# Performance work log

Hardware: AMD Instinct MI355X
Metric: run time of the kernel (lower is better)

The kernel has to match this reference:

```python
import jax, jax.numpy as jnp
import numpy as np

B, T, D, H, L = 65536, 8, 60, 128, 64


def _lstm_layer(x, Wih, Whh, bih, bhh):
    """Single LSTM layer, batch_first. x: [B,T,Din]. Returns (ys [B,T,H], h_last [B,H]).
    PyTorch gate order: i, f, g, o."""
    Bsz = x.shape[0]
    Hd = Whh.shape[1]
    # Precompute input contribution for all timesteps: [B,T,4H]
    xg = jnp.einsum('btd,gd->btg', x, Wih) + bih + bhh

    def step(carry, xt):
        h, c = carry
        g = xt + h @ Whh.T  # [B,4H]
        i, f, gg, o = jnp.split(g, 4, axis=-1)
        i = jax.nn.sigmoid(i)
        f = jax.nn.sigmoid(f)
        gg = jnp.tanh(gg)
        o = jax.nn.sigmoid(o)
        c = f * c + i * gg
        h = o * jnp.tanh(c)
        return (h, c), h

    h0 = jnp.zeros((Bsz, Hd), x.dtype)
    c0 = jnp.zeros((Bsz, Hd), x.dtype)
    (h_last, _), ys = jax.lax.scan(step, (h0, c0), jnp.swapaxes(xg, 0, 1))
    return jnp.swapaxes(ys, 0, 1), h_last


def setup_inputs() -> dict:
    key = jax.random.key(0)
    ks = jax.random.split(key, 24)
    s = 1.0 / np.sqrt(H)  # torch LSTM/Linear default uniform bound

    def u(k, shape):
        return jax.random.uniform(k, shape, jnp.float32, -s, s)

    inp = {"x": jax.random.normal(ks[0], (B, T, D), jnp.float32)}
    # encoder layer 0 (in=D), layer 1 (in=H); decoder layer 0 (in=L), layer 1 (in=H)
    dims = {"enc0": D, "enc1": H, "dec0": L, "dec1": H}
    i = 1
    for name, din in dims.items():
        inp[name + "_Wih"] = u(ks[i], (4 * H, din)); i += 1
        inp[name + "_Whh"] = u(ks[i], (4 * H, H)); i += 1
        inp[name + "_bih"] = u(ks[i], (4 * H,)); i += 1
        inp[name + "_bhh"] = u(ks[i], (4 * H,)); i += 1
    inp["W_lat"] = u(ks[i], (L, H)); i += 1
    inp["b_lat"] = u(ks[i], (L,)); i += 1
    inp["W_out"] = jax.random.uniform(ks[i], (D, H), jnp.float32, -s, s); i += 1
    inp["b_out"] = jax.random.uniform(ks[i], (D,), jnp.float32, -s, s)
    return inp


def reference(x,
              enc0_Wih, enc0_Whh, enc0_bih, enc0_bhh,
              enc1_Wih, enc1_Whh, enc1_bih, enc1_bhh,
              dec0_Wih, dec0_Whh, dec0_bih, dec0_bhh,
              dec1_Wih, dec1_Whh, dec1_bih, dec1_bhh,
              W_lat, b_lat, W_out, b_out):
    # Encoder (eval mode: inter-layer dropout is identity)
    h1, _ = _lstm_layer(x, enc0_Wih, enc0_Whh, enc0_bih, enc0_bhh)
    _, h_last = _lstm_layer(h1, enc1_Wih, enc1_Whh, enc1_bih, enc1_bhh)
    # Latent bottleneck from top-layer final hidden state
    z = h_last @ W_lat.T + b_lat  # [B,L]
    z_seq = jnp.broadcast_to(z[:, None, :], (z.shape[0], T, z.shape[1]))
    # Decoder
    d1, _ = _lstm_layer(z_seq, dec0_Wih, dec0_Whh, dec0_bih, dec0_bhh)
    d2, _ = _lstm_layer(d1, dec1_Wih, dec1_Whh, dec1_bih, dec1_bhh)
    recon = jnp.einsum('bth,dh->btd', d2, W_out) + b_out  # [B,T,D]
    return recon
```

## Files before the change

kernel.cpp:

```cpp
#include <hip/hip_runtime.h>

typedef _Float16 f16;
typedef _Float16 f16x8 __attribute__((ext_vector_type(8)));
typedef float    f32x4 __attribute__((ext_vector_type(4)));

#define MFMA16(a,b,c) __builtin_amdgcn_mfma_f32_16x16x32_f16(a,b,c,0,0,0)

#define HIST_S 1096
#define HB_S   136
#define HB_BUF 4352

__device__ __forceinline__ float sigm(float v){
  return __builtin_amdgcn_rcpf(1.f + __builtin_amdgcn_exp2f(-1.4426950408889634f*v));
}
__device__ __forceinline__ float tanha(float v){
  return 1.f - 2.f*__builtin_amdgcn_rcpf(1.f + __builtin_amdgcn_exp2f(2.8853900817779268f*v));
}
__device__ __forceinline__ f32x4 splat4(float v){ f32x4 r; r[0]=v;r[1]=v;r[2]=v;r[3]=v; return r; }

__device__ __forceinline__ f16x8 ldfrag(const float* __restrict__ W, int K, int n, int k0){
  const float* p = W + n*K + k0;
  f32x4 a = *(const f32x4*)p;
  f32x4 b = *(const f32x4*)(p+4);
  f16x8 r;
  #pragma unroll
  for (int i=0;i<4;i++){ r[i] = (f16)a[i]; r[4+i] = (f16)b[i]; }
  return r;
}
__device__ __forceinline__ f16x8 ldfrag60(const float* __restrict__ W, int n, int k0){
  const float* p = W + n*60 + k0;
  f32x4 a = *(const f32x4*)p;
  f16x8 r;
  #pragma unroll
  for (int i=0;i<4;i++) r[i] = (f16)a[i];
  if (k0 < 56){
    f32x4 b = *(const f32x4*)(p+4);
    #pragma unroll
    for (int i=0;i<4;i++) r[4+i] = (f16)b[i];
  } else {
    #pragma unroll
    for (int i=0;i<4;i++) r[4+i] = (f16)0.f;
  }
  return r;
}
__device__ __forceinline__ f16x8 zfrag(){
  f16x8 r;
  #pragma unroll
  for (int i=0;i<8;i++) r[i] = (f16)0.f;
  return r;
}

__device__ __forceinline__ void act_update(f32x4 acc[2][4], f32x4* cst, f16* dst, int stride, int col, int qd){
  #pragma unroll
  for (int m=0;m<2;m++){
    #pragma unroll
    for (int r=0;r<4;r++){
      float ii = sigm(acc[m][0][r]);
      float ff = sigm(acc[m][1][r]);
      float gg = tanha(acc[m][2][r]);
      float oo = sigm(acc[m][3][r]);
      float cn = ff*cst[m][r] + ii*gg;
      cst[m][r] = cn;
      dst[(m*16+qd*4+r)*stride + col] = (f16)(oo*tanha(cn));
    }
  }
}

__global__ void __launch_bounds__(512, 2)
lstm_main(const float* __restrict__ x,
          const float* __restrict__ e0Wih, const float* __restrict__ e0Whh, const float* __restrict__ e0bi, const float* __restrict__ e0bh,
          const float* __restrict__ e1Wih, const float* __restrict__ e1Whh, const float* __restrict__ e1bi, const float* __restrict__ e1bh,
          const float* __restrict__ d0Wih, const float* __restrict__ d0Whh, const float* __restrict__ d0bi, const float* __restrict__ d0bh,
          const float* __restrict__ d1Wih, const float* __restrict__ d1Whh, const float* __restrict__ d1bi, const float* __restrict__ d1bh,
          const float* __restrict__ Wlat,  const float* __restrict__ blat,
          const float* __restrict__ Wout,  const float* __restrict__ bout,
          float* __restrict__ out)
{
  __shared__ __align__(16) f16 hist[32*HIST_S];
  __shared__ __align__(16) f16 hb1 [HB_BUF];

  const int tid = threadIdx.x;
  const int w   = tid >> 6;
  const int ln  = tid & 15;
  const int qd  = (tid >> 4) & 3;
  const int bs  = blockIdx.x << 5;
  const int col = w*16 + ln;

  f16x8 Bf[4][8];
  f32x4 acc[2][4];
  f32x4 cst[2];
  float bg[4];

  #pragma unroll
  for (int g=0;g<4;g++){
    const int n = g*128 + col;
    #pragma unroll
    for (int kb=0;kb<2;kb++) Bf[g][kb]   = ldfrag60(e0Wih, n, kb*32 + qd*8);
    #pragma unroll
    for (int kb=0;kb<4;kb++) Bf[g][kb+2] = ldfrag(e0Whh, 128, n, kb*32 + qd*8);
    bg[g] = e0bi[n] + e0bh[n];
  }
  cst[0] = splat4(0.f); cst[1] = splat4(0.f);
  #pragma unroll 1
  for (int t=0; t<8; t++){
    #pragma unroll
    for (int m=0;m<2;m++)
      #pragma unroll
      for (int g=0;g<4;g++) acc[m][g] = splat4(bg[g]);
    #pragma unroll
    for (int kb=0; kb<2; kb++){
      #pragma unroll
      for (int m=0;m<2;m++){
        const float* p = x + (bs + m*16 + ln)*480 + t*60 + kb*32 + qd*8;
        f16x8 a;
        {
          f32x4 lo = *(const f32x4*)p;
          #pragma unroll
          for (int i=0;i<4;i++) a[i] = (f16)lo[i];
          if (kb==1 && qd==3){
            #pragma unroll
            for (int i=0;i<4;i++) a[4+i] = (f16)0.f;
          } else {
            f32x4 hi = *(const f32x4*)(p+4);
            #pragma unroll
            for (int i=0;i<4;i++) a[4+i] = (f16)hi[i];
          }
        }
        #pragma unroll
        for (int g=0; g<4; g++) acc[m][g] = MFMA16(a, Bf[g][kb], acc[m][g]);
      }
    }
    if (t > 0){
      #pragma unroll
      for (int kb=0; kb<4; kb++){
        #pragma unroll
        for (int m=0;m<2;m++){
          f16x8 a = *(const f16x8*)(hist + (m*16+ln)*HIST_S + (t-1)*HB_S + kb*32 + qd*8);
          #pragma unroll
          for (int g=0; g<4; g++) acc[m][g] = MFMA16(a, Bf[g][kb+2], acc[m][g]);
        }
      }
    }
    act_update(acc, cst, hist + t*HB_S, HIST_S, col, qd);
    __syncthreads();
  }

  #pragma unroll
  for (int g=0;g<4;g++){
    const int n = g*128 + col;
    #pragma unroll
    for (int kb=0;kb<4;kb++){
      Bf[g][kb]   = ldfrag(e1Wih, 128, n, kb*32 + qd*8);
      Bf[g][kb+4] = ldfrag(e1Whh, 128, n, kb*32 + qd*8);
    }
    bg[g] = e1bi[n] + e1bh[n];
  }
  cst[0] = splat4(0.f); cst[1] = splat4(0.f);
  #pragma unroll 1
  for (int t=0; t<8; t++){
    #pragma unroll
    for (int m=0;m<2;m++)
      #pragma unroll
      for (int g=0;g<4;g++) acc[m][g] = splat4(bg[g]);
    #pragma unroll
    for (int kb=0; kb<4; kb++){
      #pragma unroll
      for (int m=0;m<2;m++){
        f16x8 a = *(const f16x8*)(hist + (m*16+ln)*HIST_S + t*HB_S + kb*32 + qd*8);
        #pragma unroll
        for (int g=0; g<4; g++) acc[m][g] = MFMA16(a, Bf[g][kb], acc[m][g]);
      }
    }
    if (t > 0){
      #pragma unroll
      for (int kb=0; kb<4; kb++){
        #pragma unroll
        for (int m=0;m<2;m++){
          f16x8 a = *(const f16x8*)(hb1 + (m*16+ln)*HB_S + kb*32 + qd*8);
          #pragma unroll
          for (int g=0; g<4; g++) acc[m][g] = MFMA16(a, Bf[g][kb+4], acc[m][g]);
        }
      }
    }
    __syncthreads();
    act_update(acc, cst, hb1, HB_S, col, qd);
    __syncthreads();
  }

  {
    const int mo = w & 1, no = w >> 1;
    const int zn = no*16 + ln;
    f32x4 zacc = splat4(blat[zn]);
    f16x8 Bz[4];
    #pragma unroll
    for (int kb=0;kb<4;kb++) Bz[kb] = ldfrag(Wlat, 128, zn, kb*32 + qd*8);
    #pragma unroll
    for (int kb=0;kb<4;kb++){
      f16x8 a = *(const f16x8*)(hb1 + (mo*16+ln)*HB_S + kb*32 + qd*8);
      zacc = MFMA16(a, Bz[kb], zacc);
    }
    __syncthreads();
    #pragma unroll
    for (int r=0;r<4;r++)
      hb1[(mo*16+qd*4+r)*HB_S + zn] = (f16)zacc[r];
  }
  __syncthreads();

  f32x4 xga[2][4];
  {
    f16x8 Bd[4][2];
    #pragma unroll
    for (int g=0;g<4;g++){
      const int n = g*128 + col;
      #pragma unroll
      for (int kb=0;kb<2;kb++) Bd[g][kb] = ldfrag(d0Wih, 64, n, kb*32 + qd*8);
      float bgd = d0bi[n] + d0bh[n];
      xga[0][g] = splat4(bgd); xga[1][g] = splat4(bgd);
    }
    #pragma unroll
    for (int kb=0; kb<2; kb++){
      #pragma unroll
      for (int m=0;m<2;m++){
        f16x8 a = *(const f16x8*)(hb1 + (m*16+ln)*HB_S + kb*32 + qd*8);
        #pragma unroll
        for (int g=0; g<4; g++) xga[m][g] = MFMA16(a, Bd[g][kb], xga[m][g]);
      }
    }
  }

  #pragma unroll
  for (int g=0;g<4;g++){
    const int n = g*128 + col;
    #pragma unroll
    for (int kb=0;kb<4;kb++) Bf[g][kb] = ldfrag(d0Whh, 128, n, kb*32 + qd*8);
  }
  cst[0] = splat4(0.f); cst[1] = splat4(0.f);
  #pragma unroll 1
  for (int t=0; t<8; t++){
    #pragma unroll
    for (int m=0;m<2;m++)
      #pragma unroll
      for (int g=0;g<4;g++) acc[m][g] = xga[m][g];
    if (t > 0){
      #pragma unroll
      for (int kb=0; kb<4; kb++){
        #pragma unroll
        for (int m=0;m<2;m++){
          f16x8 a = *(const f16x8*)(hist + (m*16+ln)*HIST_S + (t-1)*HB_S + kb*32 + qd*8);
          #pragma unroll
          for (int g=0; g<4; g++) acc[m][g] = MFMA16(a, Bf[g][kb], acc[m][g]);
        }
      }
    }
    act_update(acc, cst, hist + t*HB_S, HIST_S, col, qd);
    __syncthreads();
  }

  #pragma unroll
  for (int g=0;g<4;g++){
    const int n = g*128 + col;
    #pragma unroll
    for (int kb=0;kb<4;kb++){
      Bf[g][kb]   = ldfrag(d1Wih, 128, n, kb*32 + qd*8);
      Bf[g][kb+4] = ldfrag(d1Whh, 128, n, kb*32 + qd*8);
    }
    bg[g] = d1bi[n] + d1bh[n];
  }
  const int dcol = (w>>1)*16 + ln;
  const int mo   = w & 1;
  f16x8 BO[4];
  #pragma unroll
  for (int kb=0;kb<4;kb++)
    BO[kb] = (dcol < 60) ? ldfrag(Wout, 128, dcol, kb*32 + qd*8) : zfrag();
  const float bo = (dcol < 60) ? bout[dcol] : 0.f;
  cst[0] = splat4(0.f); cst[1] = splat4(0.f);
  #pragma unroll 1
  for (int t=0; t<8; t++){
    #pragma unroll
    for (int m=0;m<2;m++)
      #pragma unroll
      for (int g=0;g<4;g++) acc[m][g] = splat4(bg[g]);
    #pragma unroll
    for (int kb=0; kb<4; kb++){
      #pragma unroll
      for (int m=0;m<2;m++){
        f16x8 a = *(const f16x8*)(hist + (m*16+ln)*HIST_S + t*HB_S + kb*32 + qd*8);
        #pragma unroll
        for (int g=0; g<4; g++) acc[m][g] = MFMA16(a, Bf[g][kb], acc[m][g]);
      }
    }
    if (t > 0){
      #pragma unroll
      for (int kb=0; kb<4; kb++){
        #pragma unroll
        for (int m=0;m<2;m++){
          f16x8 a = *(const f16x8*)(hb1 + (m*16+ln)*HB_S + kb*32 + qd*8);
          #pragma unroll
          for (int g=0; g<4; g++) acc[m][g] = MFMA16(a, Bf[g][kb+4], acc[m][g]);
        }
      }
    }
    __syncthreads();
    act_update(acc, cst, hb1, HB_S, col, qd);
    __syncthreads();
    f32x4 ao = splat4(bo);
    const f16* hb2 = hb1 + (mo*16+ln)*HB_S + qd*8;
    #pragma unroll
    for (int kb=0; kb<4; kb++){
      f16x8 a = *(const f16x8*)(hb2 + kb*32);
      ao = MFMA16(a, BO[kb], ao);
    }
    if (dcol < 60){
      #pragma unroll
      for (int r=0;r<4;r++){
        int s = mo*16 + qd*4 + r;
        out[(bs + s)*480 + t*60 + dcol] = ao[r];
      }
    }
  }
}

extern "C" void kernel_launch(void* const* d_in, const int* in_sizes, int n_in,
                              void* d_out, int out_size, void* d_ws, size_t ws_size,
                              hipStream_t stream)
{
  (void)d_ws; (void)ws_size; (void)in_sizes; (void)n_in; (void)out_size;
  hipLaunchKernelGGL(lstm_main, dim3(2048), dim3(512), 0, stream,
                     (const float*)d_in[0],
                     (const float*)d_in[1],  (const float*)d_in[2],  (const float*)d_in[3],  (const float*)d_in[4],
                     (const float*)d_in[5],  (const float*)d_in[6],  (const float*)d_in[7],  (const float*)d_in[8],
                     (const float*)d_in[9],  (const float*)d_in[10], (const float*)d_in[11], (const float*)d_in[12],
                     (const float*)d_in[13], (const float*)d_in[14], (const float*)d_in[15], (const float*)d_in[16],
                     (const float*)d_in[17], (const float*)d_in[18],
                     (const float*)d_in[19], (const float*)d_in[20],
                     (float*)d_out);
}
```

Baseline: 1.249 ms.

## Double rows per block and interleave stacked LSTM layers in half-sequence chunks

Each block now handles 64 batch rows instead of 32, processed in two 32-row sub-tiles so each loaded weight fragment is reused across twice as many rows. The two stacked layers of both encoder and decoder are interleaved in chunks of four timesteps, with a four-slot history buffer and a double-buffered ring for the top layer in place of a full eight-step history. The decoder's constant input projection is now recomputed every step from a latent buffer instead of being hoisted. In exchange, weights are reloaded from global memory once per half, per-thread cell state doubles, shared memory grows, and the grid is halved, which lowers the number of blocks available to fill the device.

```diff
diff --git a/kernel.cpp b/kernel.cpp
--- a/kernel.cpp
+++ b/kernel.cpp
@@ -6,9 +6,10 @@
 
 #define MFMA16(a,b,c) __builtin_amdgcn_mfma_f32_16x16x32_f16(a,b,c,0,0,0)
 
-#define HIST_S 1096
 #define HB_S   136
-#define HB_BUF 4352
+#define H4S    552
+#define RB     (64*HB_S)
+#define ZS     72
 
 __device__ __forceinline__ float sigm(float v){
   return __builtin_amdgcn_rcpf(1.f + __builtin_amdgcn_exp2f(-1.4426950408889634f*v));
@@ -50,7 +51,8 @@
   return r;
 }
 
-__device__ __forceinline__ void act_update(f32x4 acc[2][4], f32x4* cst, f16* dst, int stride, int col, int qd){
+__device__ __forceinline__ void act2(f32x4 acc[2][4], f32x4* cst, f16* dst, int stride,
+                                     int col, int qd, int mbase){
   #pragma unroll
   for (int m=0;m<2;m++){
     #pragma unroll
@@ -61,7 +63,7 @@
       float oo = sigm(acc[m][3][r]);
       float cn = ff*cst[m][r] + ii*gg;
       cst[m][r] = cn;
-      dst[(m*16+qd*4+r)*stride + col] = (f16)(oo*tanha(cn));
+      dst[((mbase+m)*16+qd*4+r)*stride + col] = (f16)(oo*tanha(cn));
     }
   }
 }
@@ -76,245 +78,272 @@
           const float* __restrict__ Wout,  const float* __restrict__ bout,
           float* __restrict__ out)
 {
-  __shared__ __align__(16) f16 hist[32*HIST_S];
-  __shared__ __align__(16) f16 hb1 [HB_BUF];
+  __shared__ __align__(16) f16 hist4[64*H4S];
+  __shared__ __align__(16) f16 ring [2*RB];
+  __shared__ __align__(16) f16 zbuf [64*ZS];
 
   const int tid = threadIdx.x;
   const int w   = tid >> 6;
   const int ln  = tid & 15;
   const int qd  = (tid >> 4) & 3;
-  const int bs  = blockIdx.x << 5;
+  const int bs  = blockIdx.x << 6;
   const int col = w*16 + ln;
 
   f16x8 Bf[4][8];
   f32x4 acc[2][4];
-  f32x4 cst[2];
+  f32x4 cstA[4], cstB[4];
   float bg[4];
 
   #pragma unroll
-  for (int g=0;g<4;g++){
-    const int n = g*128 + col;
-    #pragma unroll
-    for (int kb=0;kb<2;kb++) Bf[g][kb]   = ldfrag60(e0Wih, n, kb*32 + qd*8);
-    #pragma unroll
-    for (int kb=0;kb<4;kb++) Bf[g][kb+2] = ldfrag(e0Whh, 128, n, kb*32 + qd*8);
-    bg[g] = e0bi[n] + e0bh[n];
-  }
-  cst[0] = splat4(0.f); cst[1] = splat4(0.f);
+  for (int m=0;m<4;m++){ cstA[m] = splat4(0.f); cstB[m] = splat4(0.f); }
+
   #pragma unroll 1
-  for (int t=0; t<8; t++){
-    #pragma unroll
-    for (int m=0;m<2;m++)
-      #pragma unroll
-      for (int g=0;g<4;g++) acc[m][g] = splat4(bg[g]);
-    #pragma unroll
-    for (int kb=0; kb<2; kb++){
-      #pragma unroll
-      for (int m=0;m<2;m++){
-        const float* p = x + (bs + m*16 + ln)*480 + t*60 + kb*32 + qd*8;
-        f16x8 a;
-        {
-          f32x4 lo = *(const f32x4*)p;
-          #pragma unroll
-          for (int i=0;i<4;i++) a[i] = (f16)lo[i];
-          if (kb==1 && qd==3){
-            #pragma unroll
-            for (int i=0;i<4;i++) a[4+i] = (f16)0.f;
-          } else {
-            f32x4 hi = *(const f32x4*)(p+4);
-            #pragma unroll
-            for (int i=0;i<4;i++) a[4+i] = (f16)hi[i];
-          }
-        }
-        #pragma unroll
-        for (int g=0; g<4; g++) acc[m][g] = MFMA16(a, Bf[g][kb], acc[m][g]);
-      }
-    }
-    if (t > 0){
-      #pragma unroll
-      for (int kb=0; kb<4; kb++){
-        #pragma unroll
-        for (int m=0;m<2;m++){
-          f16x8 a = *(const f16x8*)(hist + (m*16+ln)*HIST_S + (t-1)*HB_S + kb*32 + qd*8);
-          #pragma unroll
-          for (int g=0; g<4; g++) acc[m][g] = MFMA16(a, Bf[g][kb+2], acc[m][g]);
-        }
-      }
-    }
-    act_update(acc, cst, hist + t*HB_S, HIST_S, col, qd);
-    __syncthreads();
-  }
-
-  #pragma unroll
-  for (int g=0;g<4;g++){
-    const int n = g*128 + col;
-    #pragma unroll
-    for (int kb=0;kb<4;kb++){
-      Bf[g][kb]   = ldfrag(e1Wih, 128, n, kb*32 + qd*8);
-      Bf[g][kb+4] = ldfrag(e1Whh, 128, n, kb*32 + qd*8);
-    }
-    bg[g] = e1bi[n] + e1bh[n];
-  }
-  cst[0] = splat4(0.f); cst[1] = splat4(0.f);
-  #pragma unroll 1
-  for (int t=0; t<8; t++){
-    #pragma unroll
-    for (int m=0;m<2;m++)
-      #pragma unroll
-      for (int g=0;g<4;g++) acc[m][g] = splat4(bg[g]);
-    #pragma unroll
-    for (int kb=0; kb<4; kb++){
-      #pragma unroll
-      for (int m=0;m<2;m++){
-        f16x8 a = *(const f16x8*)(hist + (m*16+ln)*HIST_S + t*HB_S + kb*32 + qd*8);
-        #pragma unroll
-        for (int g=0; g<4; g++) acc[m][g] = MFMA16(a, Bf[g][kb], acc[m][g]);
-      }
-    }
-    if (t > 0){
-      #pragma unroll
-      for (int kb=0; kb<4; kb++){
-        #pragma unroll
-        for (int m=0;m<2;m++){
-          f16x8 a = *(const f16x8*)(hb1 + (m*16+ln)*HB_S + kb*32 + qd*8);
-          #pragma unroll
-          for (int g=0; g<4; g++) acc[m][g] = MFMA16(a, Bf[g][kb+4], acc[m][g]);
-        }
-      }
-    }
-    __syncthreads();
-    act_update(acc, cst, hb1, HB_S, col, qd);
-    __syncthreads();
-  }
-
-  {
-    const int mo = w & 1, no = w >> 1;
-    const int zn = no*16 + ln;
-    f32x4 zacc = splat4(blat[zn]);
-    f16x8 Bz[4];
-    #pragma unroll
-    for (int kb=0;kb<4;kb++) Bz[kb] = ldfrag(Wlat, 128, zn, kb*32 + qd*8);
-    #pragma unroll
-    for (int kb=0;kb<4;kb++){
-      f16x8 a = *(const f16x8*)(hb1 + (mo*16+ln)*HB_S + kb*32 + qd*8);
-      zacc = MFMA16(a, Bz[kb], zacc);
-    }
-    __syncthreads();
-    #pragma unroll
-    for (int r=0;r<4;r++)
-      hb1[(mo*16+qd*4+r)*HB_S + zn] = (f16)zacc[r];
-  }
-  __syncthreads();
-
-  f32x4 xga[2][4];
-  {
-    f16x8 Bd[4][2];
+  for (int half=0; half<2; ++half){
+    const int t0 = half*4;
     #pragma unroll
     for (int g=0;g<4;g++){
       const int n = g*128 + col;
       #pragma unroll
-      for (int kb=0;kb<2;kb++) Bd[g][kb] = ldfrag(d0Wih, 64, n, kb*32 + qd*8);
-      float bgd = d0bi[n] + d0bh[n];
-      xga[0][g] = splat4(bgd); xga[1][g] = splat4(bgd);
-    }
-    #pragma unroll
-    for (int kb=0; kb<2; kb++){
-      #pragma unroll
-      for (int m=0;m<2;m++){
-        f16x8 a = *(const f16x8*)(hb1 + (m*16+ln)*HB_S + kb*32 + qd*8);
-        #pragma unroll
-        for (int g=0; g<4; g++) xga[m][g] = MFMA16(a, Bd[g][kb], xga[m][g]);
-      }
-    }
-  }
-
-  #pragma unroll
-  for (int g=0;g<4;g++){
-    const int n = g*128 + col;
-    #pragma unroll
-    for (int kb=0;kb<4;kb++) Bf[g][kb] = ldfrag(d0Whh, 128, n, kb*32 + qd*8);
-  }
-  cst[0] = splat4(0.f); cst[1] = splat4(0.f);
+      for (int kb=0;kb<2;kb++) Bf[g][kb]   = ldfrag60(e0Wih, n, kb*32 + qd*8);
+      #pragma unroll
+      for (int kb=0;kb<4;kb++) Bf[g][kb+2] = ldfrag(e0Whh, 128, n, kb*32 + qd*8);
+      bg[g] = e0bi[n] + e0bh[n];
+    }
+    #pragma unroll 1
+    for (int t=t0; t<t0+4; ++t){
+      const int slotW = (t&3)*HB_S, slotR = ((t-1)&3)*HB_S;
+      #pragma unroll
+      for (int mb=0; mb<2; ++mb){
+        #pragma unroll
+        for (int m=0;m<2;m++)
+          #pragma unroll
+          for (int g=0;g<4;g++) acc[m][g] = splat4(bg[g]);
+        #pragma unroll
+        for (int kb=0; kb<2; kb++){
+          #pragma unroll
+          for (int m=0;m<2;m++){
+            const float* p = x + (bs + (mb*2+m)*16 + ln)*480 + t*60 + kb*32 + qd*8;
+            f16x8 a;
+            f32x4 lo = *(const f32x4*)p;
+            #pragma unroll
+            for (int i=0;i<4;i++) a[i] = (f16)lo[i];
+            if (kb==1 && qd==3){
+              #pragma unroll
+              for (int i=0;i<4;i++) a[4+i] = (f16)0.f;
+            } else {
+              f32x4 hi = *(const f32x4*)(p+4);
+              #pragma unroll
+              for (int i=0;i<4;i++) a[4+i] = (f16)hi[i];
+            }
+            #pragma unroll
+            for (int g=0; g<4; g++) acc[m][g] = MFMA16(a, Bf[g][kb], acc[m][g]);
+          }
+        }
+        if (t > 0){
+          #pragma unroll
+          for (int kb=0; kb<4; kb++){
+            #pragma unroll
+            for (int m=0;m<2;m++){
+              f16x8 a = *(const f16x8*)(hist4 + ((mb*2+m)*16+ln)*H4S + slotR + kb*32 + qd*8);
+              #pragma unroll
+              for (int g=0; g<4; g++) acc[m][g] = MFMA16(a, Bf[g][kb+2], acc[m][g]);
+            }
+          }
+        }
+        act2(acc, &cstA[mb*2], hist4 + slotW, H4S, col, qd, mb*2);
+      }
+      __syncthreads();
+    }
+    #pragma unroll
+    for (int g=0;g<4;g++){
+      const int n = g*128 + col;
+      #pragma unroll
+      for (int kb=0;kb<4;kb++){
+        Bf[g][kb]   = ldfrag(e1Wih, 128, n, kb*32 + qd*8);
+        Bf[g][kb+4] = ldfrag(e1Whh, 128, n, kb*32 + qd*8);
+      }
+      bg[g] = e1bi[n] + e1bh[n];
+    }
+    #pragma unroll 1
+    for (int t=t0; t<t0+4; ++t){
+      const int slot = (t&3)*HB_S;
+      const f16* rprev = ring + ((t-1)&1)*RB;
+      f16*       rcur  = ring + (t&1)*RB;
+      #pragma unroll
+      for (int mb=0; mb<2; ++mb){
+        #pragma unroll
+        for (int m=0;m<2;m++)
+          #pragma unroll
+          for (int g=0;g<4;g++) acc[m][g] = splat4(bg[g]);
+        #pragma unroll
+        for (int kb=0; kb<4; kb++){
+          #pragma unroll
+          for (int m=0;m<2;m++){
+            f16x8 a = *(const f16x8*)(hist4 + ((mb*2+m)*16+ln)*H4S + slot + kb*32 + qd*8);
+            #pragma unroll
+            for (int g=0; g<4; g++) acc[m][g] = MFMA16(a, Bf[g][kb], acc[m][g]);
+          }
+        }
+        if (t > 0){
+          #pragma unroll
+          for (int kb=0; kb<4; kb++){
+            #pragma unroll
+            for (int m=0;m<2;m++){
+              f16x8 a = *(const f16x8*)(rprev + ((mb*2+m)*16+ln)*HB_S + kb*32 + qd*8);
+              #pragma unroll
+              for (int g=0; g<4; g++) acc[m][g] = MFMA16(a, Bf[g][kb+4], acc[m][g]);
+            }
+          }
+        }
+        act2(acc, &cstB[mb*2], rcur, HB_S, col, qd, mb*2);
+      }
+      __syncthreads();
+    }
+  }
+
+  {
+    const int mo = w & 3, nb = w >> 2;
+    const f16* r1 = ring + RB;
+    f16x8 Az[4];
+    #pragma unroll
+    for (int kb=0;kb<4;kb++)
+      Az[kb] = *(const f16x8*)(r1 + (mo*16+ln)*HB_S + kb*32 + qd*8);
+    #pragma unroll
+    for (int h2=0; h2<2; ++h2){
+      const int zn = (nb + 2*h2)*16 + ln;
+      f32x4 zacc = splat4(blat[zn]);
+      #pragma unroll
+      for (int kb=0;kb<4;kb++){
+        f16x8 Bz = ldfrag(Wlat, 128, zn, kb*32 + qd*8);
+        zacc = MFMA16(Az[kb], Bz, zacc);
+      }
+      #pragma unroll
+      for (int r=0;r<4;r++)
+        zbuf[(mo*16+qd*4+r)*ZS + zn] = (f16)zacc[r];
+    }
+    __syncthreads();
+  }
+
+  #pragma unroll
+  for (int m=0;m<4;m++){ cstA[m] = splat4(0.f); cstB[m] = splat4(0.f); }
+
+  const int mo   = w & 3;
+  const int nb   = w >> 2;
+  int  dcolH[2]; float boH[2];
+  f16x8 BO[2][4];
+  #pragma unroll
+  for (int h2=0; h2<2; ++h2){
+    dcolH[h2] = (nb + 2*h2)*16 + ln;
+    boH[h2]   = (dcolH[h2] < 60) ? bout[dcolH[h2]] : 0.f;
+    #pragma unroll
+    for (int kb=0;kb<4;kb++)
+      BO[h2][kb] = (dcolH[h2] < 60) ? ldfrag(Wout, 128, dcolH[h2], kb*32 + qd*8) : zfrag();
+  }
+
   #pragma unroll 1
-  for (int t=0; t<8; t++){
-    #pragma unroll
-    for (int m=0;m<2;m++)
-      #pragma unroll
-      for (int g=0;g<4;g++) acc[m][g] = xga[m][g];
-    if (t > 0){
-      #pragma unroll
-      for (int kb=0; kb<4; kb++){
-        #pragma unroll
-        for (int m=0;m<2;m++){
-          f16x8 a = *(const f16x8*)(hist + (m*16+ln)*HIST_S + (t-1)*HB_S + kb*32 + qd*8);
-          #pragma unroll
-          for (int g=0; g<4; g++) acc[m][g] = MFMA16(a, Bf[g][kb], acc[m][g]);
-        }
-      }
-    }
-    act_update(acc, cst, hist + t*HB_S, HIST_S, col, qd);
-    __syncthreads();
-  }
-
-  #pragma unroll
-  for (int g=0;g<4;g++){
-    const int n = g*128 + col;
-    #pragma unroll
-    for (int kb=0;kb<4;kb++){
-      Bf[g][kb]   = ldfrag(d1Wih, 128, n, kb*32 + qd*8);
-      Bf[g][kb+4] = ldfrag(d1Whh, 128, n, kb*32 + qd*8);
-    }
-    bg[g] = d1bi[n] + d1bh[n];
-  }
-  const int dcol = (w>>1)*16 + ln;
-  const int mo   = w & 1;
-  f16x8 BO[4];
-  #pragma unroll
-  for (int kb=0;kb<4;kb++)
-    BO[kb] = (dcol < 60) ? ldfrag(Wout, 128, dcol, kb*32 + qd*8) : zfrag();
-  const float bo = (dcol < 60) ? bout[dcol] : 0.f;
-  cst[0] = splat4(0.f); cst[1] = splat4(0.f);
-  #pragma unroll 1
-  for (int t=0; t<8; t++){
-    #pragma unroll
-    for (int m=0;m<2;m++)
-      #pragma unroll
-      for (int g=0;g<4;g++) acc[m][g] = splat4(bg[g]);
-    #pragma unroll
-    for (int kb=0; kb<4; kb++){
-      #pragma unroll
-      for (int m=0;m<2;m++){
-        f16x8 a = *(const f16x8*)(hist + (m*16+ln)*HIST_S + t*HB_S + kb*32 + qd*8);
-        #pragma unroll
-        for (int g=0; g<4; g++) acc[m][g] = MFMA16(a, Bf[g][kb], acc[m][g]);
-      }
-    }
-    if (t > 0){
-      #pragma unroll
-      for (int kb=0; kb<4; kb++){
-        #pragma unroll
-        for (int m=0;m<2;m++){
-          f16x8 a = *(const f16x8*)(hb1 + (m*16+ln)*HB_S + kb*32 + qd*8);
-          #pragma unroll
-          for (int g=0; g<4; g++) acc[m][g] = MFMA16(a, Bf[g][kb+4], acc[m][g]);
-        }
-      }
-    }
-    __syncthreads();
-    act_update(acc, cst, hb1, HB_S, col, qd);
-    __syncthreads();
-    f32x4 ao = splat4(bo);
-    const f16* hb2 = hb1 + (mo*16+ln)*HB_S + qd*8;
-    #pragma unroll
-    for (int kb=0; kb<4; kb++){
-      f16x8 a = *(const f16x8*)(hb2 + kb*32);
-      ao = MFMA16(a, BO[kb], ao);
-    }
-    if (dcol < 60){
-      #pragma unroll
-      for (int r=0;r<4;r++){
-        int s = mo*16 + qd*4 + r;
-        out[(bs + s)*480 + t*60 + dcol] = ao[r];
+  for (int half=0; half<2; ++half){
+    const int t0 = half*4;
+    #pragma unroll
+    for (int g=0;g<4;g++){
+      const int n = g*128 + col;
+      #pragma unroll
+      for (int kb=0;kb<2;kb++) Bf[g][kb]   = ldfrag(d0Wih, 64, n, kb*32 + qd*8);
+      #pragma unroll
+      for (int kb=0;kb<4;kb++) Bf[g][kb+2] = ldfrag(d0Whh, 128, n, kb*32 + qd*8);
+      bg[g] = d0bi[n] + d0bh[n];
+    }
+    #pragma unroll 1
+    for (int t=t0; t<t0+4; ++t){
+      const int slotW = (t&3)*HB_S, slotR = ((t-1)&3)*HB_S;
+      #pragma unroll
+      for (int mb=0; mb<2; ++mb){
+        #pragma unroll
+        for (int m=0;m<2;m++)
+          #pragma unroll
+          for (int g=0;g<4;g++) acc[m][g] = splat4(bg[g]);
+        #pragma unroll
+        for (int kb=0; kb<2; kb++){
+          #pragma unroll
+          for (int m=0;m<2;m++){
+            f16x8 a = *(const f16x8*)(zbuf + ((mb*2+m)*16+ln)*ZS + kb*32 + qd*8);
+            #pragma unroll
+            for (int g=0; g<4; g++) acc[m][g] = MFMA16(a, Bf[g][kb], acc[m][g]);
+          }
+        }
+        if (t > 0){
+          #pragma unroll
+          for (int kb=0; kb<4; kb++){
+            #pragma unroll
+            for (int m=0;m<2;m++){
+              f16x8 a = *(const f16x8*)(hist4 + ((mb*2+m)*16+ln)*H4S + slotR + kb*32 + qd*8);
+              #pragma unroll
+              for (int g=0; g<4; g++) acc[m][g] = MFMA16(a, Bf[g][kb+2], acc[m][g]);
+            }
+          }
+        }
+        act2(acc, &cstA[mb*2], hist4 + slotW, H4S, col, qd, mb*2);
+      }
+      __syncthreads();
+    }
+    #pragma unroll
+    for (int g=0;g<4;g++){
+      const int n = g*128 + col;
+      #pragma unroll
+      for (int kb=0;kb<4;kb++){
+        Bf[g][kb]   = ldfrag(d1Wih, 128, n, kb*32 + qd*8);
+        Bf[g][kb+4] = ldfrag(d1Whh, 128, n, kb*32 + qd*8);
+      }
+      bg[g] = d1bi[n] + d1bh[n];
+    }
+    #pragma unroll 1
+    for (int t=t0; t<t0+4; ++t){
+      const int slot = (t&3)*HB_S;
+      const f16* rprev = ring + ((t-1)&1)*RB;
+      f16*       rcur  = ring + (t&1)*RB;
+      #pragma unroll
+      for (int mb=0; mb<2; ++mb){
+        #pragma unroll
+        for (int m=0;m<2;m++)
+          #pragma unroll
+          for (int g=0;g<4;g++) acc[m][g] = splat4(bg[g]);
+        #pragma unroll
+        for (int kb=0; kb<4; kb++){
+          #pragma unroll
+          for (int m=0;m<2;m++){
+            f16x8 a = *(const f16x8*)(hist4 + ((mb*2+m)*16+ln)*H4S + slot + kb*32 + qd*8);
+            #pragma unroll
+            for (int g=0; g<4; g++) acc[m][g] = MFMA16(a, Bf[g][kb], acc[m][g]);
+          }
+        }
+        if (t > 0){
+          #pragma unroll
+          for (int kb=0; kb<4; kb++){
+            #pragma unroll
+            for (int m=0;m<2;m++){
+              f16x8 a = *(const f16x8*)(rprev + ((mb*2+m)*16+ln)*HB_S + kb*32 + qd*8);
+              #pragma unroll
+              for (int g=0; g<4; g++) acc[m][g] = MFMA16(a, Bf[g][kb+4], acc[m][g]);
+            }
+          }
+        }
+        act2(acc, &cstB[mb*2], rcur, HB_S, col, qd, mb*2);
+      }
+      __syncthreads();
+      #pragma unroll
+      for (int h2=0; h2<2; ++h2){
+        f32x4 ao = splat4(boH[h2]);
+        #pragma unroll
+        for (int kb=0; kb<4; kb++){
+          f16x8 a = *(const f16x8*)(rcur + (mo*16+ln)*HB_S + kb*32 + qd*8);
+          ao = MFMA16(a, BO[h2][kb], ao);
+        }
+        if (dcolH[h2] < 60){
+          #pragma unroll
+          for (int r=0;r<4;r++){
+            int s = mo*16 + qd*4 + r;
+            out[(bs + s)*480 + t*60 + dcolH[h2]] = ao[r];
+          }
+        }
       }
     }
   }
@@ -325,7 +354,7 @@
                               hipStream_t stream)
 {
   (void)d_ws; (void)ws_size; (void)in_sizes; (void)n_in; (void)out_size;
-  hipLaunchKernelGGL(lstm_main, dim3(2048), dim3(512), 0, stream,
+  hipLaunchKernelGGL(lstm_main, dim3(1024), dim3(512), 0, stream,
                      (const float*)d_in[0],
                      (const float*)d_in[1],  (const float*)d_in[2],  (const float*)d_in[3],  (const float*)d_in[4],
                      (const float*)d_in[5],  (const float*)d_in[6],  (const float*)d_in[7],  (const float*)d_in[8],
```

New measurement: 1.751 ms. +40.2%, slower.
